# Performance work log

Hardware: AMD Instinct MI355X
Metric: run time of the kernel (lower is better)

## Reference

```python
import jax, jax.numpy as jnp
import numpy as np

B, T, D = 4, 2048, 768
E, F, K = 8, 4 * 768, 2


def setup_inputs() -> dict:
    key = jax.random.key(0)
    ks = jax.random.split(key, 5)
    s = 0.02
    return {
        "x": jax.random.normal(ks[0], (B, T, D), dtype=jnp.float32),
        "Wg": jax.random.normal(ks[1], (D, E), dtype=jnp.float32) * s,
        "bg": jnp.zeros((E,), dtype=jnp.float32),
        "W1": jax.random.normal(ks[2], (E, D, F), dtype=jnp.float32) * s,
        "b1": jnp.zeros((E, F), dtype=jnp.float32),
        "W2": jax.random.normal(ks[3], (E, F, D), dtype=jnp.float32) * s,
        "b2": jnp.zeros((E, D), dtype=jnp.float32),
    }


def reference(x, Wg, bg, W1, b1, W2, b2):
    b, t, d = x.shape
    x_flat = x.reshape(-1, d)                      # [N, D]
    n = x_flat.shape[0]

    # Router: softmax over expert logits, take top-2
    gates = jax.nn.softmax(x_flat @ Wg + bg, axis=-1)   # [N, E]
    topk_g, topk_i = jax.lax.top_k(gates, K)            # [N, K]

    # Combine weights: zero for non-selected experts -> math identical to
    # masked dispatch in the torch loop (out = sum_k gate_k * expert_{idx_k}(x))
    combine = jnp.zeros((n, W1.shape[0]), dtype=gates.dtype)
    combine = combine.at[jnp.arange(n)[:, None], topk_i].add(topk_g)  # [N, E]

    # Per-expert MLP applied densely, then weighted combine (zero weights
    # kill non-selected experts' contributions)
    h = jnp.einsum('nd,edf->enf', x_flat, W1) + b1[:, None, :]  # [E, N, F]
    h = jax.nn.gelu(h, approximate=False)                        # torch nn.GELU = exact
    y = jnp.einsum('enf,efd->end', h, W2) + b2[:, None, :]       # [E, N, D]
    out = jnp.einsum('ne,end->nd', combine, y)                   # [N, D]
    return out.reshape(b, t, d)
```

## Files before the change

kernel.cpp:

```cpp
#include <hip/hip_runtime.h>
#include <hip/hip_bf16.h>


#define N_TOK 8192
#define D_DIM 768
#define E_EXP 8
#define F_DIM 3072
#define CAP   8192
#define NT_MAX 136

typedef __attribute__((ext_vector_type(8))) short s8v;
typedef __attribute__((ext_vector_type(4))) float f4v;
typedef unsigned short u16;
typedef unsigned int   u32;
typedef unsigned long long u64;

static __device__ __forceinline__ u16 f2bf(float f) {
    u32 u = __float_as_uint(f);
    return (u16)((u + 0x7fffu + ((u >> 16) & 1u)) >> 16);
}
static __device__ __forceinline__ float bf2f(u16 v) {
    return __uint_as_float((u32)v << 16);
}
static __device__ __forceinline__ float gelu_fast(float v) {
    const float av = fabsf(v);
    const float z  = av * 0.70710678118654752440f;
    const float t  = __builtin_amdgcn_rcpf(fmaf(0.3275911f, z, 1.0f));
    const float w  = __builtin_amdgcn_exp2f(-z * z * 1.4426950408889634f);
    float p = fmaf(1.061405429f, t, -1.453152027f);
    p = fmaf(p, t,  1.421413741f);
    p = fmaf(p, t, -0.284496736f);
    p = fmaf(p, t,  0.254829592f);
    p = p * t;
    const float E = 1.0f - p * w;
    return 0.5f * (v + av * E);
}
static __device__ __forceinline__ void gld_lds16(const u16* g, u16* l) {
    __builtin_amdgcn_global_load_lds(
        (const __attribute__((address_space(1))) void*)g,
        (__attribute__((address_space(3))) void*)l, 16, 0, 0);
}
template<int N> static __device__ __forceinline__ void wait_vmcnt() {
    asm volatile("s_waitcnt vmcnt(%0)" :: "n"(N) : "memory");
}
static __device__ __forceinline__ void wait_lgkm0() {
    asm volatile("s_waitcnt lgkmcnt(0)" ::: "memory");
    __builtin_amdgcn_sched_barrier(0);
}

__device__ __forceinline__ void pack_w_body(
    const float* __restrict__ src, u16* __restrict__ dst,
    int rt, int kc64, int e, int K1, int M2, int KC2, int TR, int ntm)
{
    __shared__ float ls[64][132];
    const float* se = src + (size_t)e * K1 * M2;
    const int tid = threadIdx.x;

    const int kr = tid >> 2, mq = tid & 3;
    const float* srow = se + (size_t)(kc64 * 64 + kr) * M2 + rt * 128 + mq * 32;
    #pragma unroll
    for (int it = 0; it < 8; ++it)
        *(float4*)&ls[kr][mq * 32 + it * 4] = *(const float4*)(srow + it * 4);
    __syncthreads();

    u16* dt_ = dst + ((size_t)(e * ntm + (rt * 128) / TR) * KC2 + kc64 * 2)
                     * ((size_t)TR * 32)
                   + (size_t)((rt * 128) % TR) * 32;
    const int rr = tid >> 1, hf = tid & 1;
    u16* dc = dt_ + (size_t)hf * TR * 32;
    const int row = ((rt * 128) % TR) + rr;
    #pragma unroll
    for (int j = 0; j < 4; ++j) {
        union { s8v v; u16 u[8]; } o;
        #pragma unroll
        for (int jj = 0; jj < 8; ++jj)
            o.u[jj] = f2bf(ls[hf * 32 + j * 8 + jj][rr]);
        *(s8v*)&dc[(size_t)rr * 32 + ((j ^ ((row >> 1) & 3)) * 8)] = o.v;
    }
}

__global__ __launch_bounds__(256) void prep_kernel(
    const float* __restrict__ x, const float* __restrict__ Wg,
    const float* __restrict__ bg, const float* __restrict__ W1,
    const float* __restrict__ W2, u32* __restrict__ rec_idx,
    float2* __restrict__ rec_g, u16* __restrict__ w1g,
    u16* __restrict__ w2g, int* __restrict__ counts)
{
    const int bid = blockIdx.x;
    if (bid == 0 && threadIdx.x < E_EXP) counts[threadIdx.x] = 0;

    if (bid < 2048) {
        const int wave = threadIdx.x >> 6;
        const int lane = threadIdx.x & 63;
        const int t = bid * 4 + wave;

        float acc[8];
        #pragma unroll
        for (int e = 0; e < 8; ++e) acc[e] = 0.f;

        const float* xrow = x + (size_t)t * D_DIM + lane * 12;
        #pragma unroll
        for (int i = 0; i < 3; ++i) {
            float4 xv = *(const float4*)(xrow + i * 4);
            float xs[4] = {xv.x, xv.y, xv.z, xv.w};
            #pragma unroll
            for (int j = 0; j < 4; ++j) {
                const int d = lane * 12 + i * 4 + j;
                const float4 w0 = *(const float4*)(Wg + (size_t)d * 8);
                const float4 w1 = *(const float4*)(Wg + (size_t)d * 8 + 4);
                acc[0] += xs[j] * w0.x;  acc[1] += xs[j] * w0.y;
                acc[2] += xs[j] * w0.z;  acc[3] += xs[j] * w0.w;
                acc[4] += xs[j] * w1.x;  acc[5] += xs[j] * w1.y;
                acc[6] += xs[j] * w1.z;  acc[7] += xs[j] * w1.w;
            }
        }
        #pragma unroll
        for (int e = 0; e < 8; ++e) {
            float v = acc[e];
            #pragma unroll
            for (int off = 32; off > 0; off >>= 1) v += __shfl_xor(v, off, 64);
            acc[e] = v + bg[e];
        }
        if (lane == 0) {
            float mx = acc[0];
            #pragma unroll
            for (int e = 1; e < 8; ++e) mx = fmaxf(mx, acc[e]);
            float p[8], s = 0.f;
            #pragma unroll
            for (int e = 0; e < 8; ++e) { p[e] = expf(acc[e] - mx); s += p[e]; }
            const float inv = 1.f / s;
            #pragma unroll
            for (int e = 0; e < 8; ++e) p[e] *= inv;

            int i0 = 0; float g0 = p[0];
            #pragma unroll
            for (int e = 1; e < 8; ++e) if (p[e] > g0) { g0 = p[e]; i0 = e; }
            int i1 = -1; float g1 = -1.f;
            #pragma unroll
            for (int e = 0; e < 8; ++e) if (e != i0 && p[e] > g1) { g1 = p[e]; i1 = e; }

            rec_idx[t] = (u32)i0 | ((u32)i1 << 4);
            rec_g[t] = make_float2(g0, g1);
        }
    } else if (bid < 4352) {
        const int id = bid - 2048;
        const int e = id / 288, rem = id - e * 288;
        const int rt = rem / 12, kc = rem - rt * 12;
        pack_w_body(W1, w1g, rt, kc, e, D_DIM, F_DIM, 24, 256, 12);
    } else {
        const int id = bid - 4352;
        const int e = id / 288, rem = id - e * 288;
        const int rt = rem / 48, kc = rem - rt * 48;
        pack_w_body(W2, w2g, rt, kc, e, F_DIM, D_DIM, 96, 128, 6);
    }
}

__global__ __launch_bounds__(256) void moe_scatter(
    const u32* __restrict__ rec_idx, const float2* __restrict__ rec_g,
    int* __restrict__ counts, int* __restrict__ tokbuf,
    float* __restrict__ gatebuf)
{
    const int t = blockIdx.x * 256 + threadIdx.x;
    const int lane = threadIdx.x & 63;
    const u32 pk = rec_idx[t];
    const int i0 = pk & 15, i1 = (pk >> 4) & 15;
    const float2 g = rec_g[t];
    const u64 lmask = ((u64)1 << lane) - 1;

    #pragma unroll
    for (int e = 0; e < 8; ++e) {
        const u64 m0 = __ballot(i0 == e);
        const u64 m1 = __ballot(i1 == e);
        const int c0 = __popcll(m0);
        const int total = c0 + __popcll(m1);
        if (total > 0) {
            int base = 0;
            if (lane == 0) base = atomicAdd(&counts[e], total);
            base = __shfl(base, 0, 64);
            if (i0 == e) {
                const int p = base + __popcll(m0 & lmask);
                tokbuf[(size_t)e * CAP + p] = 2 * t;
                gatebuf[(size_t)e * CAP + p] = g.x;
            }
            if (i1 == e) {
                const int p = base + c0 + __popcll(m1 & lmask);
                tokbuf[(size_t)e * CAP + p] = 2 * t + 1;
                gatebuf[(size_t)e * CAP + p] = g.y;
            }
        }
    }
}

__global__ void scan_kernel(const int* __restrict__ counts,
                            int* __restrict__ te, int* __restrict__ tb,
                            int* __restrict__ ntile) {
    if (threadIdx.x == 0) {
        int nt = 0;
        for (int e = 0; e < E_EXP; ++e)
            for (int k = 0; k * 128 < counts[e]; ++k) {
                te[nt] = e; tb[nt] = k * 128; ++nt;
            }
        *ntile = nt;
    }
}

__global__ __launch_bounds__(256) void pack_x(
    const float* __restrict__ x, const int* __restrict__ counts,
    const int* __restrict__ te, const int* __restrict__ tb,
    const int* __restrict__ ntile, const int* __restrict__ tokbuf,
    u16* __restrict__ xg)
{
    const int bx = blockIdx.x, kc = blockIdx.y;
    if (bx >= *ntile) return;
    const int e = te[bx], base = tb[bx], cnt = counts[e];
    const int tid = threadIdx.x;
    const int r = tid >> 1, hf = tid & 1;
    int ent = base + r; if (ent >= cnt) ent = cnt - 1;
    const int tok = tokbuf[(size_t)e * CAP + ent] >> 1;
    const float* xr = x + (size_t)tok * D_DIM + kc * 64 + hf * 32;
    u16* xt = xg + ((size_t)bx * 24 + kc * 2 + hf) * 4096;
    #pragma unroll
    for (int j = 0; j < 4; ++j) {
        float4 a = *(const float4*)(xr + j * 8);
        float4 b = *(const float4*)(xr + j * 8 + 4);
        union { s8v v; u16 u[8]; } o;
        o.u[0] = f2bf(a.x); o.u[1] = f2bf(a.y); o.u[2] = f2bf(a.z); o.u[3] = f2bf(a.w);
        o.u[4] = f2bf(b.x); o.u[5] = f2bf(b.y); o.u[6] = f2bf(b.z); o.u[7] = f2bf(b.w);
        *(s8v*)&xt[(size_t)r * 32 + ((j ^ ((r >> 1) & 3)) * 8)] = o.v;
    }
}

#define S1_STAGE(S, SBUF) do {                                                \
    const u16* An_ = Ab + (size_t)(S) * 8192 + w * 2048 + lane * 8;           \
    const u16* Bn_ = Bb + (size_t)(S) * 4096 + w * 1024 + lane * 8;           \
    u16* Ad_ = &Als[SBUF][w * 2048];                                          \
    u16* Bd_ = &Bls[SBUF][w * 1024];                                          \
    gld_lds16(An_,        Ad_);                                               \
    gld_lds16(An_ +  512, Ad_ +  512);                                        \
    gld_lds16(An_ + 1024, Ad_ + 1024);                                        \
    gld_lds16(An_ + 1536, Ad_ + 1536);                                        \
    gld_lds16(Bn_,        Bd_);                                               \
    gld_lds16(Bn_ +  512, Bd_ +  512);                                        \
} while (0)

#define S1_COMPUTE(BUF, VM) do {                                              \
    wait_vmcnt<VM>();                                                         \
    __builtin_amdgcn_s_barrier();                                             \
    s8v af[8], bf[4];                                                         \
    _Pragma("unroll")                                                         \
    for (int mi = 0; mi < 8; ++mi)                                            \
        af[mi] = *(const s8v*)&Als[BUF][(wm*128 + mi*16 + ln)*32 + colU];     \
    _Pragma("unroll")                                                         \
    for (int ni = 0; ni < 4; ++ni)                                            \
        bf[ni] = *(const s8v*)&Bls[BUF][(wn*64 + ni*16 + ln)*32 + colU];      \
    wait_lgkm0();                                                             \
    __builtin_amdgcn_s_barrier();                                             \
    __builtin_amdgcn_s_setprio(1);                                            \
    _Pragma("unroll")                                                         \
    for (int mi = 0; mi < 8; ++mi)                                            \
        _Pragma("unroll")                                                     \
        for (int ni = 0; ni < 4; ++ni)                                        \
            acc[mi][ni] = __builtin_amdgcn_mfma_f32_16x16x32_bf16(            \
                af[mi], bf[ni], acc[mi][ni], 0, 0, 0);                        \
    __builtin_amdgcn_s_setprio(0);                                            \
} while (0)

__global__ __launch_bounds__(256, 2) void s1_gemm(
    const u16* __restrict__ xg, const u16* __restrict__ w1g,
    const float* __restrict__ b1, const int* __restrict__ te,
    const int* __restrict__ ntile, u16* __restrict__ hg)
{
    __shared__ __align__(16) u16 Als[3][8192];
    __shared__ __align__(16) u16 Bls[3][4096];
    const int bx = blockIdx.x, by = blockIdx.y;
    if (bx >= *ntile) return;
    const int e = te[bx];

    const int tid  = threadIdx.x;
    const int w    = tid >> 6;
    const int lane = tid & 63;
    const int wm   = w & 1, wn = w >> 1;
    const int q    = lane >> 4, ln = lane & 15;
    const int colU = (q ^ ((ln >> 1) & 3)) * 8;

    const u16* Ab = w1g + (size_t)(e * 12 + by) * 24 * 8192;
    const u16* Bb = xg  + (size_t)bx * 24 * 4096;

    f4v acc[8][4];
    #pragma unroll
    for (int mi = 0; mi < 8; ++mi)
        #pragma unroll
        for (int ni = 0; ni < 4; ++ni) acc[mi][ni] = (f4v){0.f,0.f,0.f,0.f};

    S1_STAGE(0, 0);
    S1_STAGE(1, 1);

    #pragma unroll 1
    for (int k = 0; k <= 18; k += 3) {
        S1_STAGE(k + 2, 2);  S1_COMPUTE(0, 12);
        S1_STAGE(k + 3, 0);  S1_COMPUTE(1, 12);
        S1_STAGE(k + 4, 1);  S1_COMPUTE(2, 12);
    }
    S1_STAGE(23, 2);  S1_COMPUTE(0, 12);
    S1_COMPUTE(1, 6);
    S1_COMPUTE(2, 0);

    const float* b1e = b1 + (size_t)e * F_DIM + by * 256;
    #pragma unroll
    for (int mi = 0; mi < 8; ++mi) {
        const int floc = wm * 128 + mi * 16 + q * 4;
        const int kc2  = by * 8 + (floc >> 5);
        const int cg   = (floc >> 3) & 3;
        const float4 bv = *(const float4*)&b1e[floc];
        #pragma unroll
        for (int ni = 0; ni < 4; ++ni) {
            const int rr = wn * 64 + ni * 16 + ln;
            u16 us[4];
            us[0] = f2bf(gelu_fast(acc[mi][ni][0] + bv.x));
            us[1] = f2bf(gelu_fast(acc[mi][ni][1] + bv.y));
            us[2] = f2bf(gelu_fast(acc[mi][ni][2] + bv.z));
            us[3] = f2bf(gelu_fast(acc[mi][ni][3] + bv.w));
            uint2 pk;
            pk.x = (u32)us[0] | ((u32)us[1] << 16);
            pk.y = (u32)us[2] | ((u32)us[3] << 16);
            *(uint2*)&hg[((size_t)bx * 96 + kc2) * 4096 +
                         (size_t)rr * 32 + ((cg ^ ((rr >> 1) & 3)) * 8) +
                         (q & 1) * 4] = pk;
        }
    }
}

#define S2_STAGE(S, SBUF) do {                                                \
    const u16* An_ = Ab + (size_t)(S) * 4096 + w * 1024 + lane * 8;           \
    const u16* Bn_ = Bb + (size_t)(S) * 4096 + w * 1024 + lane * 8;           \
    u16* Ad_ = &Als[SBUF][w * 1024];                                          \
    u16* Bd_ = &Bls[SBUF][w * 1024];                                          \
    gld_lds16(An_,       Ad_);                                                \
    gld_lds16(An_ + 512, Ad_ + 512);                                          \
    gld_lds16(Bn_,       Bd_);                                                \
    gld_lds16(Bn_ + 512, Bd_ + 512);                                          \
} while (0)

#define S2_COMPUTE(BUF, VM) do {                                              \
    wait_vmcnt<VM>();                                                         \
    __builtin_amdgcn_s_barrier();                                             \
    s8v af[4], bf[4];                                                         \
    _Pragma("unroll")                                                         \
    for (int mi = 0; mi < 4; ++mi)                                            \
        af[mi] = *(const s8v*)&Als[BUF][(wm*64 + mi*16 + ln)*32 + colU];      \
    _Pragma("unroll")                                                         \
    for (int ni = 0; ni < 4; ++ni)                                            \
        bf[ni] = *(const s8v*)&Bls[BUF][(wn*64 + ni*16 + ln)*32 + colU];      \
    wait_lgkm0();                                                             \
    __builtin_amdgcn_s_barrier();                                             \
    __builtin_amdgcn_s_setprio(1);                                            \
    _Pragma("unroll")                                                         \
    for (int mi = 0; mi < 4; ++mi)                                            \
        _Pragma("unroll")                                                     \
        for (int ni = 0; ni < 4; ++ni)                                        \
            acc[mi][ni] = __builtin_amdgcn_mfma_f32_16x16x32_bf16(            \
                af[mi], bf[ni], acc[mi][ni], 0, 0, 0);                        \
    __builtin_amdgcn_s_setprio(0);                                            \
} while (0)

__global__ __launch_bounds__(256, 3) void s2_gemm(
    const u16* __restrict__ hg, const u16* __restrict__ w2g,
    const int* __restrict__ counts, const int* __restrict__ te,
    const int* __restrict__ tb, const int* __restrict__ ntile,
    const int* __restrict__ tokbuf, const float* __restrict__ gatebuf,
    u16* __restrict__ y)
{
    __shared__ __align__(16) u16 Als[3][4096];
    __shared__ __align__(16) u16 Bls[3][4096];
    __shared__ int   sts[128];
    __shared__ float sg[128];
    const int bx = blockIdx.x, by = blockIdx.y;
    if (bx >= *ntile) return;
    const int e = te[bx], base = tb[bx], cnt = counts[e];

    const int tid  = threadIdx.x;
    const int w    = tid >> 6;
    const int lane = tid & 63;
    const int wm   = w & 1, wn = w >> 1;
    const int q    = lane >> 4, ln = lane & 15;
    const int colU = (q ^ ((ln >> 1) & 3)) * 8;

    if (tid < 128) {
        const int ent = base + tid;
        const bool v = ent < cnt;
        sts[tid] = v ? tokbuf[(size_t)e * CAP + ent] : -1;
        sg[tid]  = v ? gatebuf[(size_t)e * CAP + ent] : 0.f;
    }

    const u16* Ab = w2g + (size_t)(e * 6 + by) * 96 * 4096;
    const u16* Bb = hg  + (size_t)bx * 96 * 4096;

    f4v acc[4][4];
    #pragma unroll
    for (int mi = 0; mi < 4; ++mi)
        #pragma unroll
        for (int ni = 0; ni < 4; ++ni) acc[mi][ni] = (f4v){0.f,0.f,0.f,0.f};

    S2_STAGE(0, 0);
    S2_STAGE(1, 1);

    #pragma unroll 1
    for (int k = 0; k <= 90; k += 3) {
        S2_STAGE(k + 2, 2);  S2_COMPUTE(0, 8);
        S2_STAGE(k + 3, 0);  S2_COMPUTE(1, 8);
        S2_STAGE(k + 4, 1);  S2_COMPUTE(2, 8);
    }
    S2_STAGE(95, 2);  S2_COMPUTE(0, 8);
    S2_COMPUTE(1, 4);
    S2_COMPUTE(2, 0);

    #pragma unroll
    for (int ni = 0; ni < 4; ++ni) {
        const int rr = wn * 64 + ni * 16 + ln;
        const int ts = sts[rr];
        if (ts >= 0) {
            const float g = sg[rr];
            u16* yr = y + (size_t)ts * D_DIM + by * 128 + wm * 64;
            #pragma unroll
            for (int mi = 0; mi < 4; ++mi) {
                u16 us[4];
                us[0] = f2bf(g * acc[mi][ni][0]);
                us[1] = f2bf(g * acc[mi][ni][1]);
                us[2] = f2bf(g * acc[mi][ni][2]);
                us[3] = f2bf(g * acc[mi][ni][3]);
                uint2 pk;
                pk.x = (u32)us[0] | ((u32)us[1] << 16);
                pk.y = (u32)us[2] | ((u32)us[3] << 16);
                *(uint2*)&yr[mi * 16 + q * 4] = pk;
            }
        }
    }
}

__global__ __launch_bounds__(256) void combine_kernel(
    const u16* __restrict__ y, const u32* __restrict__ rec_idx,
    const float2* __restrict__ rec_g, const float* __restrict__ b2,
    float* __restrict__ out)
{
    const int gid = blockIdx.x * 256 + threadIdx.x;
    const int t = gid / 192;
    const int c = (gid - t * 192) * 4;
    const u32 pk = rec_idx[t];
    const int i0 = pk & 15, i1 = (pk >> 4) & 15;
    const float2 g = rec_g[t];
    union { uint2 p; u16 u[4]; } a, b;
    a.p = *(const uint2*)&y[(size_t)(2 * t) * D_DIM + c];
    b.p = *(const uint2*)&y[(size_t)(2 * t + 1) * D_DIM + c];
    const float4 ba = *(const float4*)&b2[(size_t)i0 * D_DIM + c];
    const float4 bb = *(const float4*)&b2[(size_t)i1 * D_DIM + c];
    float4 o;
    o.x = g.x * ba.x + g.y * bb.x + bf2f(a.u[0]) + bf2f(b.u[0]);
    o.y = g.x * ba.y + g.y * bb.y + bf2f(a.u[1]) + bf2f(b.u[1]);
    o.z = g.x * ba.z + g.y * bb.z + bf2f(a.u[2]) + bf2f(b.u[2]);
    o.w = g.x * ba.w + g.y * bb.w + bf2f(a.u[3]) + bf2f(b.u[3]);
    *(float4*)&out[(size_t)t * D_DIM + c] = o;
}

extern "C" void kernel_launch(void* const* d_in, const int* in_sizes, int n_in,
                              void* d_out, int out_size, void* d_ws, size_t ws_size,
                              hipStream_t stream) {
    const float* x  = (const float*)d_in[0];
    const float* Wg = (const float*)d_in[1];
    const float* bg = (const float*)d_in[2];
    const float* W1 = (const float*)d_in[3];
    const float* b1 = (const float*)d_in[4];
    const float* W2 = (const float*)d_in[5];
    const float* b2 = (const float*)d_in[6];
    float* out = (float*)d_out;

    char* ws = (char*)d_ws;
    size_t off = 0;
    u16* xg  = (u16*)(ws + off); off += (size_t)NT_MAX * 24 * 4096 * sizeof(u16);
    u16* w1g = (u16*)(ws + off); off += (size_t)E_EXP * F_DIM * D_DIM * sizeof(u16);
    u16* w2g = (u16*)(ws + off); off += (size_t)E_EXP * D_DIM * F_DIM * sizeof(u16);
    u16* hg  = (u16*)(ws + off); off += (size_t)NT_MAX * 96 * 4096 * sizeof(u16);
    u16* y   = (u16*)(ws + off); off += (size_t)2 * N_TOK * D_DIM * sizeof(u16);
    int* tokbuf = (int*)(ws + off);      off += (size_t)E_EXP * CAP * sizeof(int);
    float* gatebuf = (float*)(ws + off); off += (size_t)E_EXP * CAP * sizeof(float);
    u32* rec_idx = (u32*)(ws + off);     off += (size_t)N_TOK * sizeof(u32);
    float2* rec_g = (float2*)(ws + off); off += (size_t)N_TOK * sizeof(float2);
    int* counts = (int*)(ws + off);      off += 64;
    int* te     = (int*)(ws + off);      off += NT_MAX * sizeof(int);
    int* tb     = (int*)(ws + off);      off += NT_MAX * sizeof(int);
    int* ntile  = (int*)(ws + off);      off += 64;

    prep_kernel<<<6656, 256, 0, stream>>>(x, Wg, bg, W1, W2, rec_idx, rec_g,
                                          w1g, w2g, counts);
    moe_scatter<<<N_TOK / 256, 256, 0, stream>>>(rec_idx, rec_g, counts, tokbuf, gatebuf);
    scan_kernel<<<1, 64, 0, stream>>>(counts, te, tb, ntile);
    pack_x<<<dim3(NT_MAX, 12), 256, 0, stream>>>(x, counts, te, tb, ntile, tokbuf, xg);

    s1_gemm<<<dim3(NT_MAX, 12), 256, 0, stream>>>(xg, w1g, b1, te, ntile, hg);
    s2_gemm<<<dim3(NT_MAX, 6), 256, 0, stream>>>(hg, w2g, counts, te, tb, ntile,
                                                 tokbuf, gatebuf, y);
    combine_kernel<<<(N_TOK * 192) / 256, 256, 0, stream>>>(y, rec_idx, rec_g, b2, out);
}
```

Baseline: 509.0 us.

## Enlarge s2 GEMM tile to 256x128 sharing s1 pipeline; use packed bf16 convert

```diff
diff --git a/kernel.cpp b/kernel.cpp
--- a/kernel.cpp
+++ b/kernel.cpp
@@ -21,6 +21,11 @@
 }
 static __device__ __forceinline__ float bf2f(u16 v) {
     return __uint_as_float((u32)v << 16);
+}
+static __device__ __forceinline__ u32 cvt_pk_bf16(float lo, float hi) {
+    u32 r;
+    asm("v_cvt_pk_bf16_f32 %0, %1, %2" : "=v"(r) : "v"(lo), "v"(hi));
+    return r;
 }
 static __device__ __forceinline__ float gelu_fast(float v) {
     const float av = fabsf(v);
@@ -151,7 +156,7 @@
         const int id = bid - 4352;
         const int e = id / 288, rem = id - e * 288;
         const int rt = rem / 48, kc = rem - rt * 48;
-        pack_w_body(W2, w2g, rt, kc, e, F_DIM, D_DIM, 96, 128, 6);
+        pack_w_body(W2, w2g, rt, kc, e, F_DIM, D_DIM, 96, 256, 3);
     }
 }
 
@@ -230,7 +235,7 @@
     }
 }
 
-#define S1_STAGE(S, SBUF) do {                                                \
+#define G_STAGE(S, SBUF) do {                                                 \
     const u16* An_ = Ab + (size_t)(S) * 8192 + w * 2048 + lane * 8;           \
     const u16* Bn_ = Bb + (size_t)(S) * 4096 + w * 1024 + lane * 8;           \
     u16* Ad_ = &Als[SBUF][w * 2048];                                          \
@@ -243,7 +248,7 @@
     gld_lds16(Bn_ +  512, Bd_ +  512);                                        \
 } while (0)
 
-#define S1_COMPUTE(BUF, VM) do {                                              \
+#define G_COMPUTE(BUF, VM) do {                                               \
     wait_vmcnt<VM>();                                                         \
     __builtin_amdgcn_s_barrier();                                             \
     s8v af[8], bf[4];                                                         \
@@ -292,18 +297,18 @@
         #pragma unroll
         for (int ni = 0; ni < 4; ++ni) acc[mi][ni] = (f4v){0.f,0.f,0.f,0.f};
 
-    S1_STAGE(0, 0);
-    S1_STAGE(1, 1);
+    G_STAGE(0, 0);
+    G_STAGE(1, 1);
 
     #pragma unroll 1
     for (int k = 0; k <= 18; k += 3) {
-        S1_STAGE(k + 2, 2);  S1_COMPUTE(0, 12);
-        S1_STAGE(k + 3, 0);  S1_COMPUTE(1, 12);
-        S1_STAGE(k + 4, 1);  S1_COMPUTE(2, 12);
-    }
-    S1_STAGE(23, 2);  S1_COMPUTE(0, 12);
-    S1_COMPUTE(1, 6);
-    S1_COMPUTE(2, 0);
+        G_STAGE(k + 2, 2);  G_COMPUTE(0, 12);
+        G_STAGE(k + 3, 0);  G_COMPUTE(1, 12);
+        G_STAGE(k + 4, 1);  G_COMPUTE(2, 12);
+    }
+    G_STAGE(23, 2);  G_COMPUTE(0, 12);
+    G_COMPUTE(1, 6);
+    G_COMPUTE(2, 0);
 
     const float* b1e = b1 + (size_t)e * F_DIM + by * 256;
     #pragma unroll
@@ -315,14 +320,11 @@
         #pragma unroll
         for (int ni = 0; ni < 4; ++ni) {
             const int rr = wn * 64 + ni * 16 + ln;
-            u16 us[4];
-            us[0] = f2bf(gelu_fast(acc[mi][ni][0] + bv.x));
-            us[1] = f2bf(gelu_fast(acc[mi][ni][1] + bv.y));
-            us[2] = f2bf(gelu_fast(acc[mi][ni][2] + bv.z));
-            us[3] = f2bf(gelu_fast(acc[mi][ni][3] + bv.w));
             uint2 pk;
-            pk.x = (u32)us[0] | ((u32)us[1] << 16);
-            pk.y = (u32)us[2] | ((u32)us[3] << 16);
+            pk.x = cvt_pk_bf16(gelu_fast(acc[mi][ni][0] + bv.x),
+                               gelu_fast(acc[mi][ni][1] + bv.y));
+            pk.y = cvt_pk_bf16(gelu_fast(acc[mi][ni][2] + bv.z),
+                               gelu_fast(acc[mi][ni][3] + bv.w));
             *(uint2*)&hg[((size_t)bx * 96 + kc2) * 4096 +
                          (size_t)rr * 32 + ((cg ^ ((rr >> 1) & 3)) * 8) +
                          (q & 1) * 4] = pk;
@@ -330,47 +332,14 @@
     }
 }
 
-#define S2_STAGE(S, SBUF) do {                                                \
-    const u16* An_ = Ab + (size_t)(S) * 4096 + w * 1024 + lane * 8;           \
-    const u16* Bn_ = Bb + (size_t)(S) * 4096 + w * 1024 + lane * 8;           \
-    u16* Ad_ = &Als[SBUF][w * 1024];                                          \
-    u16* Bd_ = &Bls[SBUF][w * 1024];                                          \
-    gld_lds16(An_,       Ad_);                                                \
-    gld_lds16(An_ + 512, Ad_ + 512);                                          \
-    gld_lds16(Bn_,       Bd_);                                                \
-    gld_lds16(Bn_ + 512, Bd_ + 512);                                          \
-} while (0)
-
-#define S2_COMPUTE(BUF, VM) do {                                              \
-    wait_vmcnt<VM>();                                                         \
-    __builtin_amdgcn_s_barrier();                                             \
-    s8v af[4], bf[4];                                                         \
-    _Pragma("unroll")                                                         \
-    for (int mi = 0; mi < 4; ++mi)                                            \
-        af[mi] = *(const s8v*)&Als[BUF][(wm*64 + mi*16 + ln)*32 + colU];      \
-    _Pragma("unroll")                                                         \
-    for (int ni = 0; ni < 4; ++ni)                                            \
-        bf[ni] = *(const s8v*)&Bls[BUF][(wn*64 + ni*16 + ln)*32 + colU];      \
-    wait_lgkm0();                                                             \
-    __builtin_amdgcn_s_barrier();                                             \
-    __builtin_amdgcn_s_setprio(1);                                            \
-    _Pragma("unroll")                                                         \
-    for (int mi = 0; mi < 4; ++mi)                                            \
-        _Pragma("unroll")                                                     \
-        for (int ni = 0; ni < 4; ++ni)                                        \
-            acc[mi][ni] = __builtin_amdgcn_mfma_f32_16x16x32_bf16(            \
-                af[mi], bf[ni], acc[mi][ni], 0, 0, 0);                        \
-    __builtin_amdgcn_s_setprio(0);                                            \
-} while (0)
-
-__global__ __launch_bounds__(256, 3) void s2_gemm(
+__global__ __launch_bounds__(256, 2) void s2_gemm(
     const u16* __restrict__ hg, const u16* __restrict__ w2g,
     const int* __restrict__ counts, const int* __restrict__ te,
     const int* __restrict__ tb, const int* __restrict__ ntile,
     const int* __restrict__ tokbuf, const float* __restrict__ gatebuf,
     u16* __restrict__ y)
 {
-    __shared__ __align__(16) u16 Als[3][4096];
+    __shared__ __align__(16) u16 Als[3][8192];
     __shared__ __align__(16) u16 Bls[3][4096];
     __shared__ int   sts[128];
     __shared__ float sg[128];
@@ -392,27 +361,27 @@
         sg[tid]  = v ? gatebuf[(size_t)e * CAP + ent] : 0.f;
     }
 
-    const u16* Ab = w2g + (size_t)(e * 6 + by) * 96 * 4096;
+    const u16* Ab = w2g + (size_t)(e * 3 + by) * 96 * 8192;
     const u16* Bb = hg  + (size_t)bx * 96 * 4096;
 
-    f4v acc[4][4];
-    #pragma unroll
-    for (int mi = 0; mi < 4; ++mi)
+    f4v acc[8][4];
+    #pragma unroll
+    for (int mi = 0; mi < 8; ++mi)
         #pragma unroll
         for (int ni = 0; ni < 4; ++ni) acc[mi][ni] = (f4v){0.f,0.f,0.f,0.f};
 
-    S2_STAGE(0, 0);
-    S2_STAGE(1, 1);
+    G_STAGE(0, 0);
+    G_STAGE(1, 1);
 
     #pragma unroll 1
     for (int k = 0; k <= 90; k += 3) {
-        S2_STAGE(k + 2, 2);  S2_COMPUTE(0, 8);
-        S2_STAGE(k + 3, 0);  S2_COMPUTE(1, 8);
-        S2_STAGE(k + 4, 1);  S2_COMPUTE(2, 8);
-    }
-    S2_STAGE(95, 2);  S2_COMPUTE(0, 8);
-    S2_COMPUTE(1, 4);
-    S2_COMPUTE(2, 0);
+        G_STAGE(k + 2, 2);  G_COMPUTE(0, 12);
+        G_STAGE(k + 3, 0);  G_COMPUTE(1, 12);
+        G_STAGE(k + 4, 1);  G_COMPUTE(2, 12);
+    }
+    G_STAGE(95, 2);  G_COMPUTE(0, 12);
+    G_COMPUTE(1, 6);
+    G_COMPUTE(2, 0);
 
     #pragma unroll
     for (int ni = 0; ni < 4; ++ni) {
@@ -420,18 +389,13 @@
         const int ts = sts[rr];
         if (ts >= 0) {
             const float g = sg[rr];
-            u16* yr = y + (size_t)ts * D_DIM + by * 128 + wm * 64;
-            #pragma unroll
-            for (int mi = 0; mi < 4; ++mi) {
-                u16 us[4];
-                us[0] = f2bf(g * acc[mi][ni][0]);
-                us[1] = f2bf(g * acc[mi][ni][1]);
-                us[2] = f2bf(g * acc[mi][ni][2]);
-                us[3] = f2bf(g * acc[mi][ni][3]);
+            u16* yr = y + (size_t)ts * D_DIM + by * 256 + wm * 128 + q * 4;
+            #pragma unroll
+            for (int mi = 0; mi < 8; ++mi) {
                 uint2 pk;
-                pk.x = (u32)us[0] | ((u32)us[1] << 16);
-                pk.y = (u32)us[2] | ((u32)us[3] << 16);
-                *(uint2*)&yr[mi * 16 + q * 4] = pk;
+                pk.x = cvt_pk_bf16(g * acc[mi][ni][0], g * acc[mi][ni][1]);
+                pk.y = cvt_pk_bf16(g * acc[mi][ni][2], g * acc[mi][ni][3]);
+                *(uint2*)&yr[mi * 16] = pk;
             }
         }
     }
@@ -496,7 +460,7 @@
     pack_x<<<dim3(NT_MAX, 12), 256, 0, stream>>>(x, counts, te, tb, ntile, tokbuf, xg);
 
     s1_gemm<<<dim3(NT_MAX, 12), 256, 0, stream>>>(xg, w1g, b1, te, ntile, hg);
-    s2_gemm<<<dim3(NT_MAX, 6), 256, 0, stream>>>(hg, w2g, counts, te, tb, ntile,
+    s2_gemm<<<dim3(NT_MAX, 3), 256, 0, stream>>>(hg, w2g, counts, te, tb, ntile,
                                                  tokbuf, gatebuf, y);
     combine_kernel<<<(N_TOK * 192) / 256, 256, 0, stream>>>(y, rec_idx, rec_g, b2, out);
 }
```

Measured after the change: 510.9 us. No clear change (+0.4%).
